# Performance work log

Hardware: AMD Instinct MI355X
Metric: run time of the kernel (lower is better)

Reference implementation:

```python
import jax, jax.numpy as jnp
import numpy as np

T, B, D, H, O = 512, 64, 512, 1024, 512

def _xavier(key, shape):
    fan_out, fan_in = shape
    limit = np.sqrt(6.0 / (fan_in + fan_out))
    return jax.random.uniform(key, shape, jnp.float32, -limit, limit)

def setup_inputs() -> dict:
    key = jax.random.key(0)
    ks = jax.random.split(key, 10)
    x = jax.random.normal(ks[0], (T, B, D), jnp.float32)
    # Gate order: i, f, o, c (stacked along first axis for a fused 4H projection;
    # math identical to 8 separate Linears in the torch module, biases init to 0
    # but we randomize them slightly for a non-trivial reference).
    Wx = jnp.concatenate([_xavier(ks[1 + g], (H, D)) for g in range(4)], axis=0)  # [4H, D]
    Wh = jnp.concatenate([_xavier(ks[5 + g], (H, H)) for g in range(4)], axis=0)  # [4H, H]
    bx = jnp.zeros((4 * H,), jnp.float32)
    bh = jnp.zeros((4 * H,), jnp.float32)
    Why = _xavier(ks[9], (O, H))
    bhy = jnp.zeros((O,), jnp.float32)
    return {"x": x, "Wx": Wx, "bx": bx, "Wh": Wh, "bh": bh, "Why": Why, "bhy": bhy}

def reference(x, Wx, bx, Wh, bh, Why, bhy):
    Hd = Wh.shape[1]
    Bd = x.shape[1]
    # Precompute all input-path projections in one batched GEMM: [T, B, 4H]
    xp = jnp.einsum('tbd,gd->tbg', x, Wx) + bx + bh

    def step(carry, xp_t):
        h, c = carry
        gates = xp_t + h @ Wh.T  # [B, 4H]
        i_t = jax.nn.sigmoid(gates[:, 0 * Hd:1 * Hd])
        f_t = jax.nn.sigmoid(gates[:, 1 * Hd:2 * Hd])
        o_t = jax.nn.sigmoid(gates[:, 2 * Hd:3 * Hd])
        c_tilde = jnp.tanh(gates[:, 3 * Hd:4 * Hd])
        c = f_t * c + i_t * c_tilde
        h = o_t * jnp.tanh(c)
        return (h, c), None

    h0 = jnp.zeros((Bd, Hd), x.dtype)
    c0 = jnp.zeros((Bd, Hd), x.dtype)
    (h, c), _ = jax.lax.scan(step, (h0, c0), xp)
    return h @ Why.T + bhy  # [B, O]
```

## Files before the change

kernel.cpp:

```cpp
#include <hip/hip_runtime.h>
#include <hip/hip_bf16.h>
#include <math.h>

constexpr int T = 512;
constexpr int B = 64;
constexpr int D = 512;
constexpr int H = 1024;
constexpr int O = 512;
constexpr int GROUPS = 2;
constexpr int BG   = B / GROUPS;
constexpr int GBLK = 128;
constexpr int COLS = 32;
constexpr int KCH  = (D + H) / 8;

typedef __attribute__((ext_vector_type(8))) __bf16 bf16x8;
typedef __attribute__((ext_vector_type(4))) float  floatx4;

struct GBar {
    unsigned arr[GBLK];
};

__global__ __launch_bounds__(256) void convert_w(
    const float* __restrict__ Wx, const float* __restrict__ Wh,
    __bf16* __restrict__ Wc)
{
    const int id = blockIdx.x * 256 + threadIdx.x;
    if (id >= GBLK * KCH * COLS) return;
    const int nl     = id & 31;
    const int kchunk = (id >> 5) % KCH;
    const int strip  = id / (KCH * COLS);
    const int s  = nl >> 4;
    const int jl = (nl >> 2) & 3;
    const int g  = nl & 3;
    const int j  = strip * 8 + 2 * jl + s;
    const int k0 = kchunk * 8;
    const float* src = (k0 < D) ? &Wx[(size_t)(g * H + j) * D + k0]
                                : &Wh[(size_t)(g * H + j) * H + (k0 - D)];
    const float4 a = *(const float4*)src;
    const float4 b = *(const float4*)(src + 4);
    __bf16 t8[8] = {(__bf16)a.x,(__bf16)a.y,(__bf16)a.z,(__bf16)a.w,
                    (__bf16)b.x,(__bf16)b.y,(__bf16)b.z,(__bf16)b.w};
    *(uint4*)&Wc[(size_t)id * 8] = *(uint4*)t8;
}

__global__ __launch_bounds__(256) void make_bias(
    const float* __restrict__ bx, const float* __restrict__ bh,
    float* __restrict__ bias)
{
    const int n = blockIdx.x * 256 + threadIdx.x;
    if (n < 4 * H) {
        const int gbn = n >> 5, nl = n & 31;
        const int s  = nl >> 4;
        const int jl = (nl >> 2) & 3;
        const int g  = nl & 3;
        const int j  = gbn * 8 + 2 * jl + s;
        bias[n] = bx[g * H + j] + bh[g * H + j];
    }
}

__global__ __launch_bounds__(128, 1) void lstm_persistent(
    const float* __restrict__ x,
    const __bf16* __restrict__ Wc,
    const float* __restrict__ bias,
    __bf16* __restrict__ hbufs,
    float* __restrict__ hfin,
    GBar* bars)
{
    __shared__ __attribute__((aligned(16))) __bf16 wlds[KCH * COLS * 8];

    const int tid   = threadIdx.x;
    const int wid   = tid >> 6;
    const int lane  = tid & 63;
    const int cm    = lane & 15;
    const int q     = lane >> 4;
    const int group = blockIdx.x >> 7;
    const int gb    = blockIdx.x & 127;
    const int n0    = gb * COLS;
    GBar* bar = bars + group;
    __bf16* hb0 = hbufs + (size_t)group * 2 * BG * H;
    __bf16* hb1 = hb0 + BG * H;

    {
        const uint4* wsrc = (const uint4*)(Wc + (size_t)gb * KCH * COLS * 8);
        uint4* wdst = (uint4*)wlds;
        for (int i = tid; i < KCH * COLS; i += 128) wdst[i] = wsrc[i];
    }
    const int p4 = cm & 3;
    const int jl = cm >> 2;
    const int row_l = wid * 16 + q * 4 + p4;
    const float4 bias0q = *(const float4*)&bias[n0 + jl * 4];
    const float4 bias1q = *(const float4*)&bias[n0 + 16 + jl * 4];
    float c0 = 0.f, c1 = 0.f;
    __syncthreads();

    const int grow = group * BG + wid * 16 + cm;
    const float* xrow = x + (size_t)grow * D + q * 8;
    const int    hoff = (wid * 16 + cm) * H + q * 8;
    const __bf16* wl  = wlds + (q * 32 + cm) * 8;
    const unsigned* fa = bar->arr + 2 * lane;

    floatx4 acc[2][2];
    float4  xcur[16][2];

    auto loadx = [&](int tt) {
        const float* xr = xrow + (size_t)tt * (B * D);
        #pragma unroll
        for (int s = 0; s < 16; ++s) {
            xcur[s][0] = *(const float4*)(xr + s * 32);
            xcur[s][1] = *(const float4*)(xr + s * 32 + 4);
        }
    };
    auto xmfma = [&]() {
        acc[0][0] = (floatx4){0,0,0,0}; acc[0][1] = (floatx4){0,0,0,0};
        acc[1][0] = (floatx4){0,0,0,0}; acc[1][1] = (floatx4){0,0,0,0};
        #pragma unroll
        for (int s = 0; s < 16; ++s) {
            const float4 a0 = xcur[s][0], a1 = xcur[s][1];
            const bf16x8 af = {(__bf16)a0.x,(__bf16)a0.y,(__bf16)a0.z,(__bf16)a0.w,
                               (__bf16)a1.x,(__bf16)a1.y,(__bf16)a1.z,(__bf16)a1.w};
            const bf16x8 b0 = *(const bf16x8*)(wl + s * 1024);
            const bf16x8 b1 = *(const bf16x8*)(wl + s * 1024 + 128);
            acc[0][s & 1] = __builtin_amdgcn_mfma_f32_16x16x32_bf16(af, b0, acc[0][s & 1], 0, 0, 0);
            acc[1][s & 1] = __builtin_amdgcn_mfma_f32_16x16x32_bf16(af, b1, acc[1][s & 1], 0, 0, 0);
        }
    };

    auto quadT = [&](float v[4]) {
        float w0 = __shfl_xor(v[1], 1), w1 = __shfl_xor(v[0], 1);
        float w2 = __shfl_xor(v[3], 1), w3 = __shfl_xor(v[2], 1);
        if (p4 & 1) { v[0] = w0; v[2] = w2; } else { v[1] = w1; v[3] = w3; }
        w0 = __shfl_xor(v[2], 2); w1 = __shfl_xor(v[3], 2);
        w2 = __shfl_xor(v[0], 2); w3 = __shfl_xor(v[1], 2);
        if (p4 & 2) { v[0] = w0; v[1] = w1; } else { v[2] = w2; v[3] = w3; }
    };

    loadx(0);
    xmfma();

    for (int t = 0; t < T; ++t) {
        const __bf16* hcur = (t & 1) ? hb1 : hb0;
        __bf16*       hnxt = (t & 1) ? hb0 : hb1;

        {
            const __bf16* hbase = hcur + hoff;
            uint4 hv[32];
            unsigned f0t, f1t;
            asm volatile(
                "1: global_load_dword %[f0], %[fa], off sc0 sc1\n\t"
                "global_load_dword %[f1], %[fa], off offset:4 sc0 sc1\n\t"
                "s_waitcnt vmcnt(0)\n\t"
                "v_min_i32 %[f0], %[f0], %[f1]\n\t"
                "v_cmp_gt_i32 vcc, %[tt], %[f0]\n\t"
                "s_cbranch_vccz 2f\n\t"
                "s_sleep 1\n\t"
                "s_branch 1b\n\t"
                "2: global_load_dwordx4 %[h0], %[hb], off sc0 sc1\n\t"
                "global_load_dwordx4 %[h1], %[hb], off offset:64 sc0 sc1\n\t"
                "global_load_dwordx4 %[h2], %[hb], off offset:128 sc0 sc1\n\t"
                "global_load_dwordx4 %[h3], %[hb], off offset:192 sc0 sc1\n\t"
                "global_load_dwordx4 %[h4], %[hb], off offset:256 sc0 sc1\n\t"
                "global_load_dwordx4 %[h5], %[hb], off offset:320 sc0 sc1\n\t"
                "global_load_dwordx4 %[h6], %[hb], off offset:384 sc0 sc1\n\t"
                "global_load_dwordx4 %[h7], %[hb], off offset:448 sc0 sc1\n\t"
                "global_load_dwordx4 %[h8], %[hb], off offset:512 sc0 sc1\n\t"
                "global_load_dwordx4 %[h9], %[hb], off offset:576 sc0 sc1\n\t"
                "global_load_dwordx4 %[h10], %[hb], off offset:640 sc0 sc1\n\t"
                "global_load_dwordx4 %[h11], %[hb], off offset:704 sc0 sc1\n\t"
                "global_load_dwordx4 %[h12], %[hb], off offset:768 sc0 sc1\n\t"
                "global_load_dwordx4 %[h13], %[hb], off offset:832 sc0 sc1\n\t"
                "global_load_dwordx4 %[h14], %[hb], off offset:896 sc0 sc1\n\t"
                "global_load_dwordx4 %[h15], %[hb], off offset:960 sc0 sc1\n\t"
                "global_load_dwordx4 %[h16], %[hb], off offset:1024 sc0 sc1\n\t"
                "global_load_dwordx4 %[h17], %[hb], off offset:1088 sc0 sc1\n\t"
                "global_load_dwordx4 %[h18], %[hb], off offset:1152 sc0 sc1\n\t"
                "global_load_dwordx4 %[h19], %[hb], off offset:1216 sc0 sc1\n\t"
                "global_load_dwordx4 %[h20], %[hb], off offset:1280 sc0 sc1\n\t"
                "global_load_dwordx4 %[h21], %[hb], off offset:1344 sc0 sc1\n\t"
                "global_load_dwordx4 %[h22], %[hb], off offset:1408 sc0 sc1\n\t"
                "global_load_dwordx4 %[h23], %[hb], off offset:1472 sc0 sc1\n\t"
                "global_load_dwordx4 %[h24], %[hb], off offset:1536 sc0 sc1\n\t"
                "global_load_dwordx4 %[h25], %[hb], off offset:1600 sc0 sc1\n\t"
                "global_load_dwordx4 %[h26], %[hb], off offset:1664 sc0 sc1\n\t"
                "global_load_dwordx4 %[h27], %[hb], off offset:1728 sc0 sc1\n\t"
                "global_load_dwordx4 %[h28], %[hb], off offset:1792 sc0 sc1\n\t"
                "global_load_dwordx4 %[h29], %[hb], off offset:1856 sc0 sc1\n\t"
                "global_load_dwordx4 %[h30], %[hb], off offset:1920 sc0 sc1\n\t"
                "global_load_dwordx4 %[h31], %[hb], off offset:1984 sc0 sc1\n\t"
                "s_waitcnt vmcnt(0)"
                : [h0]"=&v"(hv[0]),  [h1]"=&v"(hv[1]),  [h2]"=&v"(hv[2]),  [h3]"=&v"(hv[3]),
                  [h4]"=&v"(hv[4]),  [h5]"=&v"(hv[5]),  [h6]"=&v"(hv[6]),  [h7]"=&v"(hv[7]),
                  [h8]"=&v"(hv[8]),  [h9]"=&v"(hv[9]),  [h10]"=&v"(hv[10]), [h11]"=&v"(hv[11]),
                  [h12]"=&v"(hv[12]), [h13]"=&v"(hv[13]), [h14]"=&v"(hv[14]), [h15]"=&v"(hv[15]),
                  [h16]"=&v"(hv[16]), [h17]"=&v"(hv[17]), [h18]"=&v"(hv[18]), [h19]"=&v"(hv[19]),
                  [h20]"=&v"(hv[20]), [h21]"=&v"(hv[21]), [h22]"=&v"(hv[22]), [h23]"=&v"(hv[23]),
                  [h24]"=&v"(hv[24]), [h25]"=&v"(hv[25]), [h26]"=&v"(hv[26]), [h27]"=&v"(hv[27]),
                  [h28]"=&v"(hv[28]), [h29]"=&v"(hv[29]), [h30]"=&v"(hv[30]), [h31]"=&v"(hv[31]),
                  [f0]"=&v"(f0t), [f1]"=&v"(f1t)
                : [hb]"v"(hbase), [fa]"v"(fa), [tt]"v"(t)
                : "memory", "vcc");
            #pragma unroll
            for (int sg = 0; sg < 32; ++sg) {
                union { uint4 u; bf16x8 v; } hf; hf.u = hv[sg];
                const bf16x8 b0 = *(const bf16x8*)(wl + 16384 + sg * 1024);
                const bf16x8 b1 = *(const bf16x8*)(wl + 16384 + sg * 1024 + 128);
                acc[0][sg & 1] = __builtin_amdgcn_mfma_f32_16x16x32_bf16(hf.v, b0, acc[0][sg & 1], 0, 0, 0);
                acc[1][sg & 1] = __builtin_amdgcn_mfma_f32_16x16x32_bf16(hf.v, b1, acc[1][sg & 1], 0, 0, 0);
            }
        }
        const floatx4 av0 = acc[0][0] + acc[0][1];
        const floatx4 av1 = acc[1][0] + acc[1][1];

        float g0v[4] = {av0.x, av0.y, av0.z, av0.w};
        float g1v[4] = {av1.x, av1.y, av1.z, av1.w};
        quadT(g0v);
        quadT(g1v);

        if (t + 1 < T) loadx(t + 1);

        const float i0 = 1.f / (1.f + expf(-(g0v[0] + bias0q.x)));
        const float f0 = 1.f / (1.f + expf(-(g0v[1] + bias0q.y)));
        const float o0 = 1.f / (1.f + expf(-(g0v[2] + bias0q.z)));
        const float t0 = tanhf(g0v[3] + bias0q.w);
        const float i1 = 1.f / (1.f + expf(-(g1v[0] + bias1q.x)));
        const float f1 = 1.f / (1.f + expf(-(g1v[1] + bias1q.y)));
        const float o1 = 1.f / (1.f + expf(-(g1v[2] + bias1q.z)));
        const float t1 = tanhf(g1v[3] + bias1q.w);
        c0 = f0 * c0 + i0 * t0;
        c1 = f1 * c1 + i1 * t1;
        const float hv0 = o0 * tanhf(c0);
        const float hv1 = o1 * tanhf(c1);
        const int j0 = gb * 8 + 2 * jl;
        const int hi = row_l * H + j0;
        union { __bf16 h2[2]; unsigned u; } hp;
        hp.h2[0] = (__bf16)hv0; hp.h2[1] = (__bf16)hv1;
        __hip_atomic_store((unsigned*)&hnxt[hi], hp.u, __ATOMIC_RELAXED,
                           __HIP_MEMORY_SCOPE_AGENT);
        if (t == T - 1) {
            const int gr = group * BG + row_l;
            hfin[gr * H + j0]     = hv0;
            hfin[gr * H + j0 + 1] = hv1;
        }

        __syncthreads();

        if (tid == 0)
            __hip_atomic_store(&bar->arr[gb], (unsigned)(t + 1),
                               __ATOMIC_RELAXED, __HIP_MEMORY_SCOPE_AGENT);

        if (t + 1 < T) xmfma();
    }
}

__global__ __launch_bounds__(256) void out_gemm(
    const float* __restrict__ h, const float* __restrict__ Why,
    const float* __restrict__ bhy, float* __restrict__ out)
{
    const int idx = blockIdx.x * 256 + threadIdx.x;
    if (idx >= B * O) return;
    const int b = idx / O;
    const int o = idx % O;
    const float4* hv = (const float4*)&h[(size_t)b * H];
    const float4* wv = (const float4*)&Why[(size_t)o * H];
    float s = 0.f;
    #pragma unroll 4
    for (int k = 0; k < H / 4; ++k) {
        const float4 a = hv[k];
        const float4 w = wv[k];
        s += a.x * w.x + a.y * w.y + a.z * w.z + a.w * w.w;
    }
    out[idx] = s + bhy[o];
}

extern "C" void kernel_launch(void* const* d_in, const int* in_sizes, int n_in,
                              void* d_out, int out_size, void* d_ws, size_t ws_size,
                              hipStream_t stream) {
    const float* x   = (const float*)d_in[0];
    const float* Wx  = (const float*)d_in[1];
    const float* bx  = (const float*)d_in[2];
    const float* Wh  = (const float*)d_in[3];
    const float* bh  = (const float*)d_in[4];
    const float* Why = (const float*)d_in[5];
    const float* bhy = (const float*)d_in[6];
    float* out = (float*)d_out;

    char* ws = (char*)d_ws;
    __bf16* Wc    = (__bf16*)ws;
    float*  bias  = (float*)(ws + 12582912);
    __bf16* hbufs = (__bf16*)(ws + 12599296);
    GBar*   bars  = (GBar*)  (ws + 12861440);
    float*  hfin  = (float*)ws;

    (void)hipMemsetAsync(ws + 12599296, 0, 262144 + 2 * sizeof(GBar), stream);
    convert_w<<<3072, 256, 0, stream>>>(Wx, Wh, Wc);
    make_bias<<<16, 256, 0, stream>>>(bx, bh, bias);

    lstm_persistent<<<GROUPS * GBLK, 128, 0, stream>>>(x, Wc, bias, hbufs,
                                                       hfin, bars);

    out_gemm<<<(B * O + 255) / 256, 256, 0, stream>>>(hfin, Why, bhy, out);
}
```

Measured before the change: 3.198 ms.

## Widen persistent LSTM blocks to 64 columns, keep only Wh in LDS

Halves the number of persistent blocks per group (128 to 64) and doubles the hidden columns each block owns, so each h tile loaded per step feeds four MFMAs instead of two. Only the recurrent Wh slice (128 KB) is kept in LDS, and the input-projection weights are read from global memory each step. The barrier poll drops to one flag per lane and h is stored as 64-bit packed bf16. The final fp32 h copy is removed and the output GEMM reads the bf16 ping-pong buffer instead, which trades precision for skipping that write. Risks include global weight traffic in xmfma, higher per-block work, and the output reading a bf16 rather than fp32 hidden state.

```diff
diff --git a/kernel.cpp b/kernel.cpp
--- a/kernel.cpp
+++ b/kernel.cpp
@@ -9,8 +9,8 @@
 constexpr int O = 512;
 constexpr int GROUPS = 2;
 constexpr int BG   = B / GROUPS;
-constexpr int GBLK = 128;
-constexpr int COLS = 32;
+constexpr int GBLK = 64;
+constexpr int COLS = 64;
 constexpr int KCH  = (D + H) / 8;
 
 typedef __attribute__((ext_vector_type(8))) __bf16 bf16x8;
@@ -25,14 +25,14 @@
     __bf16* __restrict__ Wc)
 {
     const int id = blockIdx.x * 256 + threadIdx.x;
-    if (id >= GBLK * KCH * COLS) return;
-    const int nl     = id & 31;
-    const int kchunk = (id >> 5) % KCH;
-    const int strip  = id / (KCH * COLS);
-    const int s  = nl >> 4;
-    const int jl = (nl >> 2) & 3;
-    const int g  = nl & 3;
-    const int j  = strip * 8 + 2 * jl + s;
+    if (id >= GBLK * KCH * 64) return;
+    const int nl6    = id & 63;
+    const int kchunk = (id >> 6) % KCH;
+    const int blk    = id / (KCH * 64);
+    const int s  = nl6 >> 4;
+    const int jl = (nl6 >> 2) & 3;
+    const int g  = nl6 & 3;
+    const int j  = blk * 16 + jl * 4 + s;
     const int k0 = kchunk * 8;
     const float* src = (k0 < D) ? &Wx[(size_t)(g * H + j) * D + k0]
                                 : &Wh[(size_t)(g * H + j) * H + (k0 - D)];
@@ -49,11 +49,11 @@
 {
     const int n = blockIdx.x * 256 + threadIdx.x;
     if (n < 4 * H) {
-        const int gbn = n >> 5, nl = n & 31;
-        const int s  = nl >> 4;
-        const int jl = (nl >> 2) & 3;
-        const int g  = nl & 3;
-        const int j  = gbn * 8 + 2 * jl + s;
+        const int gbn = n >> 6, nl6 = n & 63;
+        const int s  = nl6 >> 4;
+        const int jl = (nl6 >> 2) & 3;
+        const int g  = nl6 & 3;
+        const int j  = gbn * 16 + jl * 4 + s;
         bias[n] = bx[g * H + j] + bh[g * H + j];
     }
 }
@@ -63,43 +63,45 @@
     const __bf16* __restrict__ Wc,
     const float* __restrict__ bias,
     __bf16* __restrict__ hbufs,
-    float* __restrict__ hfin,
     GBar* bars)
 {
-    __shared__ __attribute__((aligned(16))) __bf16 wlds[KCH * COLS * 8];
+    __shared__ __attribute__((aligned(16))) __bf16 wlds[128 * 512];
 
     const int tid   = threadIdx.x;
     const int wid   = tid >> 6;
     const int lane  = tid & 63;
     const int cm    = lane & 15;
     const int q     = lane >> 4;
-    const int group = blockIdx.x >> 7;
-    const int gb    = blockIdx.x & 127;
+    const int group = blockIdx.x >> 6;
+    const int gb    = blockIdx.x & 63;
     const int n0    = gb * COLS;
     GBar* bar = bars + group;
     __bf16* hb0 = hbufs + (size_t)group * 2 * BG * H;
     __bf16* hb1 = hb0 + BG * H;
 
     {
-        const uint4* wsrc = (const uint4*)(Wc + (size_t)gb * KCH * COLS * 8);
+        const uint4* wsrc = (const uint4*)(Wc + ((size_t)gb * KCH + 64) * 512);
         uint4* wdst = (uint4*)wlds;
-        for (int i = tid; i < KCH * COLS; i += 128) wdst[i] = wsrc[i];
+        for (int i = tid; i < 8192; i += 128) wdst[i] = wsrc[i];
     }
     const int p4 = cm & 3;
     const int jl = cm >> 2;
     const int row_l = wid * 16 + q * 4 + p4;
-    const float4 bias0q = *(const float4*)&bias[n0 + jl * 4];
-    const float4 bias1q = *(const float4*)&bias[n0 + 16 + jl * 4];
-    float c0 = 0.f, c1 = 0.f;
+    float4 biasq[4];
+    #pragma unroll
+    for (int s = 0; s < 4; ++s)
+        biasq[s] = *(const float4*)&bias[n0 + s * 16 + jl * 4];
+    float cst[4] = {0.f, 0.f, 0.f, 0.f};
     __syncthreads();
 
     const int grow = group * BG + wid * 16 + cm;
     const float* xrow = x + (size_t)grow * D + q * 8;
     const int    hoff = (wid * 16 + cm) * H + q * 8;
-    const __bf16* wl  = wlds + (q * 32 + cm) * 8;
-    const unsigned* fa = bar->arr + 2 * lane;
-
-    floatx4 acc[2][2];
+    const __bf16* wl  = wlds + q * 512 + cm * 8;
+    const __bf16* wxg = Wc + (size_t)gb * KCH * 512 + q * 512 + cm * 8;
+    const unsigned* fa = bar->arr + lane;
+
+    floatx4 acc[4];
     float4  xcur[16][2];
 
     auto loadx = [&](int tt) {
@@ -111,17 +113,18 @@
         }
     };
     auto xmfma = [&]() {
-        acc[0][0] = (floatx4){0,0,0,0}; acc[0][1] = (floatx4){0,0,0,0};
-        acc[1][0] = (floatx4){0,0,0,0}; acc[1][1] = (floatx4){0,0,0,0};
+        acc[0] = (floatx4){0,0,0,0}; acc[1] = (floatx4){0,0,0,0};
+        acc[2] = (floatx4){0,0,0,0}; acc[3] = (floatx4){0,0,0,0};
         #pragma unroll
-        for (int s = 0; s < 16; ++s) {
-            const float4 a0 = xcur[s][0], a1 = xcur[s][1];
+        for (int s16 = 0; s16 < 16; ++s16) {
+            const float4 a0 = xcur[s16][0], a1 = xcur[s16][1];
             const bf16x8 af = {(__bf16)a0.x,(__bf16)a0.y,(__bf16)a0.z,(__bf16)a0.w,
                                (__bf16)a1.x,(__bf16)a1.y,(__bf16)a1.z,(__bf16)a1.w};
-            const bf16x8 b0 = *(const bf16x8*)(wl + s * 1024);
-            const bf16x8 b1 = *(const bf16x8*)(wl + s * 1024 + 128);
-            acc[0][s & 1] = __builtin_amdgcn_mfma_f32_16x16x32_bf16(af, b0, acc[0][s & 1], 0, 0, 0);
-            acc[1][s & 1] = __builtin_amdgcn_mfma_f32_16x16x32_bf16(af, b1, acc[1][s & 1], 0, 0, 0);
+            #pragma unroll
+            for (int s = 0; s < 4; ++s) {
+                const bf16x8 b = *(const bf16x8*)(wxg + s16 * 2048 + s * 128);
+                acc[s] = __builtin_amdgcn_mfma_f32_16x16x32_bf16(af, b, acc[s], 0, 0, 0);
+            }
         }
     };
 
@@ -144,12 +147,10 @@
         {
             const __bf16* hbase = hcur + hoff;
             uint4 hv[32];
-            unsigned f0t, f1t;
+            unsigned f0t;
             asm volatile(
                 "1: global_load_dword %[f0], %[fa], off sc0 sc1\n\t"
-                "global_load_dword %[f1], %[fa], off offset:4 sc0 sc1\n\t"
                 "s_waitcnt vmcnt(0)\n\t"
-                "v_min_i32 %[f0], %[f0], %[f1]\n\t"
                 "v_cmp_gt_i32 vcc, %[tt], %[f0]\n\t"
                 "s_cbranch_vccz 2f\n\t"
                 "s_sleep 1\n\t"
@@ -195,51 +196,46 @@
                   [h20]"=&v"(hv[20]), [h21]"=&v"(hv[21]), [h22]"=&v"(hv[22]), [h23]"=&v"(hv[23]),
                   [h24]"=&v"(hv[24]), [h25]"=&v"(hv[25]), [h26]"=&v"(hv[26]), [h27]"=&v"(hv[27]),
                   [h28]"=&v"(hv[28]), [h29]"=&v"(hv[29]), [h30]"=&v"(hv[30]), [h31]"=&v"(hv[31]),
-                  [f0]"=&v"(f0t), [f1]"=&v"(f1t)
+                  [f0]"=&v"(f0t)
                 : [hb]"v"(hbase), [fa]"v"(fa), [tt]"v"(t)
                 : "memory", "vcc");
             #pragma unroll
             for (int sg = 0; sg < 32; ++sg) {
                 union { uint4 u; bf16x8 v; } hf; hf.u = hv[sg];
-                const bf16x8 b0 = *(const bf16x8*)(wl + 16384 + sg * 1024);
-                const bf16x8 b1 = *(const bf16x8*)(wl + 16384 + sg * 1024 + 128);
-                acc[0][sg & 1] = __builtin_amdgcn_mfma_f32_16x16x32_bf16(hf.v, b0, acc[0][sg & 1], 0, 0, 0);
-                acc[1][sg & 1] = __builtin_amdgcn_mfma_f32_16x16x32_bf16(hf.v, b1, acc[1][sg & 1], 0, 0, 0);
+                #pragma unroll
+                for (int s = 0; s < 4; ++s) {
+                    const bf16x8 b = *(const bf16x8*)(wl + sg * 2048 + s * 128);
+                    acc[s] = __builtin_amdgcn_mfma_f32_16x16x32_bf16(hf.v, b, acc[s], 0, 0, 0);
+                }
             }
         }
-        const floatx4 av0 = acc[0][0] + acc[0][1];
-        const floatx4 av1 = acc[1][0] + acc[1][1];
-
-        float g0v[4] = {av0.x, av0.y, av0.z, av0.w};
-        float g1v[4] = {av1.x, av1.y, av1.z, av1.w};
-        quadT(g0v);
-        quadT(g1v);
+
+        float gv[4][4];
+        #pragma unroll
+        for (int s = 0; s < 4; ++s) {
+            gv[s][0] = acc[s].x; gv[s][1] = acc[s].y;
+            gv[s][2] = acc[s].z; gv[s][3] = acc[s].w;
+            quadT(gv[s]);
+        }
 
         if (t + 1 < T) loadx(t + 1);
 
-        const float i0 = 1.f / (1.f + expf(-(g0v[0] + bias0q.x)));
-        const float f0 = 1.f / (1.f + expf(-(g0v[1] + bias0q.y)));
-        const float o0 = 1.f / (1.f + expf(-(g0v[2] + bias0q.z)));
-        const float t0 = tanhf(g0v[3] + bias0q.w);
-        const float i1 = 1.f / (1.f + expf(-(g1v[0] + bias1q.x)));
-        const float f1 = 1.f / (1.f + expf(-(g1v[1] + bias1q.y)));
-        const float o1 = 1.f / (1.f + expf(-(g1v[2] + bias1q.z)));
-        const float t1 = tanhf(g1v[3] + bias1q.w);
-        c0 = f0 * c0 + i0 * t0;
-        c1 = f1 * c1 + i1 * t1;
-        const float hv0 = o0 * tanhf(c0);
-        const float hv1 = o1 * tanhf(c1);
-        const int j0 = gb * 8 + 2 * jl;
+        __bf16 hq[4];
+        #pragma unroll
+        for (int s = 0; s < 4; ++s) {
+            const float ig = 1.f / (1.f + expf(-(gv[s][0] + biasq[s].x)));
+            const float fg = 1.f / (1.f + expf(-(gv[s][1] + biasq[s].y)));
+            const float og = 1.f / (1.f + expf(-(gv[s][2] + biasq[s].z)));
+            const float ct = tanhf(gv[s][3] + biasq[s].w);
+            cst[s] = fg * cst[s] + ig * ct;
+            hq[s] = (__bf16)(og * tanhf(cst[s]));
+        }
+        const int j0 = gb * 16 + jl * 4;
         const int hi = row_l * H + j0;
-        union { __bf16 h2[2]; unsigned u; } hp;
-        hp.h2[0] = (__bf16)hv0; hp.h2[1] = (__bf16)hv1;
-        __hip_atomic_store((unsigned*)&hnxt[hi], hp.u, __ATOMIC_RELAXED,
-                           __HIP_MEMORY_SCOPE_AGENT);
-        if (t == T - 1) {
-            const int gr = group * BG + row_l;
-            hfin[gr * H + j0]     = hv0;
-            hfin[gr * H + j0 + 1] = hv1;
-        }
+        union { __bf16 h4[4]; unsigned long long u; } hp;
+        hp.h4[0] = hq[0]; hp.h4[1] = hq[1]; hp.h4[2] = hq[2]; hp.h4[3] = hq[3];
+        __hip_atomic_store((unsigned long long*)&hnxt[hi], hp.u,
+                           __ATOMIC_RELAXED, __HIP_MEMORY_SCOPE_AGENT);
 
         __syncthreads();
 
@@ -252,21 +248,27 @@
 }
 
 __global__ __launch_bounds__(256) void out_gemm(
-    const float* __restrict__ h, const float* __restrict__ Why,
+    const __bf16* __restrict__ hbufs, const float* __restrict__ Why,
     const float* __restrict__ bhy, float* __restrict__ out)
 {
     const int idx = blockIdx.x * 256 + threadIdx.x;
     if (idx >= B * O) return;
     const int b = idx / O;
     const int o = idx % O;
-    const float4* hv = (const float4*)&h[(size_t)b * H];
+    const int group = b >> 5, row_l = b & 31;
+    const __bf16* hb = hbufs + (size_t)group * 2 * BG * H + (size_t)row_l * H;
     const float4* wv = (const float4*)&Why[(size_t)o * H];
     float s = 0.f;
     #pragma unroll 4
-    for (int k = 0; k < H / 4; ++k) {
-        const float4 a = hv[k];
-        const float4 w = wv[k];
-        s += a.x * w.x + a.y * w.y + a.z * w.z + a.w * w.w;
+    for (int k8 = 0; k8 < H / 8; ++k8) {
+        union { uint4 u; bf16x8 v; } hh;
+        hh.u = ((const uint4*)hb)[k8];
+        const float4 w0 = wv[2 * k8];
+        const float4 w1 = wv[2 * k8 + 1];
+        s += (float)hh.v[0] * w0.x + (float)hh.v[1] * w0.y +
+             (float)hh.v[2] * w0.z + (float)hh.v[3] * w0.w +
+             (float)hh.v[4] * w1.x + (float)hh.v[5] * w1.y +
+             (float)hh.v[6] * w1.z + (float)hh.v[7] * w1.w;
     }
     out[idx] = s + bhy[o];
 }
@@ -288,14 +290,13 @@
     float*  bias  = (float*)(ws + 12582912);
     __bf16* hbufs = (__bf16*)(ws + 12599296);
     GBar*   bars  = (GBar*)  (ws + 12861440);
-    float*  hfin  = (float*)ws;
 
     (void)hipMemsetAsync(ws + 12599296, 0, 262144 + 2 * sizeof(GBar), stream);
     convert_w<<<3072, 256, 0, stream>>>(Wx, Wh, Wc);
     make_bias<<<16, 256, 0, stream>>>(bx, bh, bias);
 
     lstm_persistent<<<GROUPS * GBLK, 128, 0, stream>>>(x, Wc, bias, hbufs,
-                                                       hfin, bars);
-
-    out_gemm<<<(B * O + 255) / 256, 256, 0, stream>>>(hfin, Why, bhy, out);
-}
+                                                       bars);
+
+    out_gemm<<<(B * O + 255) / 256, 256, 0, stream>>>(hbufs, Why, bhy, out);
+}
```

New measurement: 8.778 ms. 2.75x slower.

## Elect per-XCD leader block to poll barrier and relay readiness locally

Applied to the files above, without the earlier changes.

One block per XCD and group becomes a leader. Only the leaders poll the global step barrier, then they acquire-fence and publish a per-XCD flag. The other blocks on that XCD spin on the flag, and then load h with sc0 only, so the loads can hit the XCD's L2 instead of bypassing it. The aim is to cut cross-die barrier polling traffic and the cost of system-coherent h loads, in exchange for an extra hop in the signalling chain. Correctness depends on the non-leader's sc0 loads seeing fresh h data in L2 after the leader's fence, which may not be guaranteed without invalidation.

```diff
diff --git a/kernel.cpp b/kernel.cpp
--- a/kernel.cpp
+++ b/kernel.cpp
@@ -64,9 +64,12 @@
     const float* __restrict__ bias,
     __bf16* __restrict__ hbufs,
     float* __restrict__ hfin,
-    GBar* bars)
+    GBar* bars,
+    unsigned* invFlag,
+    unsigned* xcdCnt)
 {
     __shared__ __attribute__((aligned(16))) __bf16 wlds[KCH * COLS * 8];
+    __shared__ int sLead, sSlot;
 
     const int tid   = threadIdx.x;
     const int wid   = tid >> 6;
@@ -80,10 +83,18 @@
     __bf16* hb0 = hbufs + (size_t)group * 2 * BG * H;
     __bf16* hb1 = hb0 + BG * H;
 
+    unsigned xcd;
+    asm volatile("s_getreg_b32 %0, hwreg(HW_REG_XCC_ID)" : "=s"(xcd));
+
     {
         const uint4* wsrc = (const uint4*)(Wc + (size_t)gb * KCH * COLS * 8);
         uint4* wdst = (uint4*)wlds;
         for (int i = tid; i < KCH * COLS; i += 128) wdst[i] = wsrc[i];
+    }
+    if (tid == 0) {
+        const int slot = ((int)(xcd & 7)) * 2 + group;
+        sSlot = slot;
+        sLead = (atomicAdd(&xcdCnt[slot], 1u) == 0);
     }
     const int p4 = cm & 3;
     const int jl = cm >> 2;
@@ -92,6 +103,8 @@
     const float4 bias1q = *(const float4*)&bias[n0 + 16 + jl * 4];
     float c0 = 0.f, c1 = 0.f;
     __syncthreads();
+    const int isLead = sLead;
+    unsigned* ivf = invFlag + sSlot * 16;
 
     const int grow = group * BG + wid * 16 + cm;
     const float* xrow = x + (size_t)grow * D + q * 8;
@@ -140,10 +153,9 @@
     for (int t = 0; t < T; ++t) {
         const __bf16* hcur = (t & 1) ? hb1 : hb0;
         __bf16*       hnxt = (t & 1) ? hb0 : hb1;
-
-        {
-            const __bf16* hbase = hcur + hoff;
-            uint4 hv[32];
+        const __bf16* hbase = hcur + hoff;
+
+        if (isLead) {
             unsigned f0t, f1t;
             asm volatile(
                 "1: global_load_dword %[f0], %[fa], off sc0 sc1\n\t"
@@ -154,38 +166,64 @@
                 "s_cbranch_vccz 2f\n\t"
                 "s_sleep 1\n\t"
                 "s_branch 1b\n\t"
-                "2: global_load_dwordx4 %[h0], %[hb], off sc0 sc1\n\t"
-                "global_load_dwordx4 %[h1], %[hb], off offset:64 sc0 sc1\n\t"
-                "global_load_dwordx4 %[h2], %[hb], off offset:128 sc0 sc1\n\t"
-                "global_load_dwordx4 %[h3], %[hb], off offset:192 sc0 sc1\n\t"
-                "global_load_dwordx4 %[h4], %[hb], off offset:256 sc0 sc1\n\t"
-                "global_load_dwordx4 %[h5], %[hb], off offset:320 sc0 sc1\n\t"
-                "global_load_dwordx4 %[h6], %[hb], off offset:384 sc0 sc1\n\t"
-                "global_load_dwordx4 %[h7], %[hb], off offset:448 sc0 sc1\n\t"
-                "global_load_dwordx4 %[h8], %[hb], off offset:512 sc0 sc1\n\t"
-                "global_load_dwordx4 %[h9], %[hb], off offset:576 sc0 sc1\n\t"
-                "global_load_dwordx4 %[h10], %[hb], off offset:640 sc0 sc1\n\t"
-                "global_load_dwordx4 %[h11], %[hb], off offset:704 sc0 sc1\n\t"
-                "global_load_dwordx4 %[h12], %[hb], off offset:768 sc0 sc1\n\t"
-                "global_load_dwordx4 %[h13], %[hb], off offset:832 sc0 sc1\n\t"
-                "global_load_dwordx4 %[h14], %[hb], off offset:896 sc0 sc1\n\t"
-                "global_load_dwordx4 %[h15], %[hb], off offset:960 sc0 sc1\n\t"
-                "global_load_dwordx4 %[h16], %[hb], off offset:1024 sc0 sc1\n\t"
-                "global_load_dwordx4 %[h17], %[hb], off offset:1088 sc0 sc1\n\t"
-                "global_load_dwordx4 %[h18], %[hb], off offset:1152 sc0 sc1\n\t"
-                "global_load_dwordx4 %[h19], %[hb], off offset:1216 sc0 sc1\n\t"
-                "global_load_dwordx4 %[h20], %[hb], off offset:1280 sc0 sc1\n\t"
-                "global_load_dwordx4 %[h21], %[hb], off offset:1344 sc0 sc1\n\t"
-                "global_load_dwordx4 %[h22], %[hb], off offset:1408 sc0 sc1\n\t"
-                "global_load_dwordx4 %[h23], %[hb], off offset:1472 sc0 sc1\n\t"
-                "global_load_dwordx4 %[h24], %[hb], off offset:1536 sc0 sc1\n\t"
-                "global_load_dwordx4 %[h25], %[hb], off offset:1600 sc0 sc1\n\t"
-                "global_load_dwordx4 %[h26], %[hb], off offset:1664 sc0 sc1\n\t"
-                "global_load_dwordx4 %[h27], %[hb], off offset:1728 sc0 sc1\n\t"
-                "global_load_dwordx4 %[h28], %[hb], off offset:1792 sc0 sc1\n\t"
-                "global_load_dwordx4 %[h29], %[hb], off offset:1856 sc0 sc1\n\t"
-                "global_load_dwordx4 %[h30], %[hb], off offset:1920 sc0 sc1\n\t"
-                "global_load_dwordx4 %[h31], %[hb], off offset:1984 sc0 sc1\n\t"
+                "2:"
+                : [f0]"=&v"(f0t), [f1]"=&v"(f1t)
+                : [fa]"v"(fa), [tt]"v"(t)
+                : "memory", "vcc");
+            __builtin_amdgcn_fence(__ATOMIC_ACQUIRE, "agent");
+            if (tid == 0)
+                __hip_atomic_store(&ivf[0], (unsigned)(t + 1),
+                                   __ATOMIC_RELAXED, __HIP_MEMORY_SCOPE_AGENT);
+        } else {
+            unsigned f0t;
+            asm volatile(
+                "1: global_load_dword %[f0], %[iv], off sc0 sc1\n\t"
+                "s_waitcnt vmcnt(0)\n\t"
+                "v_cmp_gt_u32 vcc, %[t1], %[f0]\n\t"
+                "s_cbranch_vccz 2f\n\t"
+                "s_sleep 1\n\t"
+                "s_branch 1b\n\t"
+                "2:"
+                : [f0]"=&v"(f0t)
+                : [iv]"v"(ivf), [t1]"v"(t + 1)
+                : "memory", "vcc");
+        }
+
+        {
+            uint4 hv[32];
+            asm volatile(
+                "global_load_dwordx4 %[h0], %[hb], off sc0\n\t"
+                "global_load_dwordx4 %[h1], %[hb], off offset:64 sc0\n\t"
+                "global_load_dwordx4 %[h2], %[hb], off offset:128 sc0\n\t"
+                "global_load_dwordx4 %[h3], %[hb], off offset:192 sc0\n\t"
+                "global_load_dwordx4 %[h4], %[hb], off offset:256 sc0\n\t"
+                "global_load_dwordx4 %[h5], %[hb], off offset:320 sc0\n\t"
+                "global_load_dwordx4 %[h6], %[hb], off offset:384 sc0\n\t"
+                "global_load_dwordx4 %[h7], %[hb], off offset:448 sc0\n\t"
+                "global_load_dwordx4 %[h8], %[hb], off offset:512 sc0\n\t"
+                "global_load_dwordx4 %[h9], %[hb], off offset:576 sc0\n\t"
+                "global_load_dwordx4 %[h10], %[hb], off offset:640 sc0\n\t"
+                "global_load_dwordx4 %[h11], %[hb], off offset:704 sc0\n\t"
+                "global_load_dwordx4 %[h12], %[hb], off offset:768 sc0\n\t"
+                "global_load_dwordx4 %[h13], %[hb], off offset:832 sc0\n\t"
+                "global_load_dwordx4 %[h14], %[hb], off offset:896 sc0\n\t"
+                "global_load_dwordx4 %[h15], %[hb], off offset:960 sc0\n\t"
+                "global_load_dwordx4 %[h16], %[hb], off offset:1024 sc0\n\t"
+                "global_load_dwordx4 %[h17], %[hb], off offset:1088 sc0\n\t"
+                "global_load_dwordx4 %[h18], %[hb], off offset:1152 sc0\n\t"
+                "global_load_dwordx4 %[h19], %[hb], off offset:1216 sc0\n\t"
+                "global_load_dwordx4 %[h20], %[hb], off offset:1280 sc0\n\t"
+                "global_load_dwordx4 %[h21], %[hb], off offset:1344 sc0\n\t"
+                "global_load_dwordx4 %[h22], %[hb], off offset:1408 sc0\n\t"
+                "global_load_dwordx4 %[h23], %[hb], off offset:1472 sc0\n\t"
+                "global_load_dwordx4 %[h24], %[hb], off offset:1536 sc0\n\t"
+                "global_load_dwordx4 %[h25], %[hb], off offset:1600 sc0\n\t"
+                "global_load_dwordx4 %[h26], %[hb], off offset:1664 sc0\n\t"
+                "global_load_dwordx4 %[h27], %[hb], off offset:1728 sc0\n\t"
+                "global_load_dwordx4 %[h28], %[hb], off offset:1792 sc0\n\t"
+                "global_load_dwordx4 %[h29], %[hb], off offset:1856 sc0\n\t"
+                "global_load_dwordx4 %[h30], %[hb], off offset:1920 sc0\n\t"
+                "global_load_dwordx4 %[h31], %[hb], off offset:1984 sc0\n\t"
                 "s_waitcnt vmcnt(0)"
                 : [h0]"=&v"(hv[0]),  [h1]"=&v"(hv[1]),  [h2]"=&v"(hv[2]),  [h3]"=&v"(hv[3]),
                   [h4]"=&v"(hv[4]),  [h5]"=&v"(hv[5]),  [h6]"=&v"(hv[6]),  [h7]"=&v"(hv[7]),
@@ -194,10 +232,9 @@
                   [h16]"=&v"(hv[16]), [h17]"=&v"(hv[17]), [h18]"=&v"(hv[18]), [h19]"=&v"(hv[19]),
                   [h20]"=&v"(hv[20]), [h21]"=&v"(hv[21]), [h22]"=&v"(hv[22]), [h23]"=&v"(hv[23]),
                   [h24]"=&v"(hv[24]), [h25]"=&v"(hv[25]), [h26]"=&v"(hv[26]), [h27]"=&v"(hv[27]),
-                  [h28]"=&v"(hv[28]), [h29]"=&v"(hv[29]), [h30]"=&v"(hv[30]), [h31]"=&v"(hv[31]),
-                  [f0]"=&v"(f0t), [f1]"=&v"(f1t)
-                : [hb]"v"(hbase), [fa]"v"(fa), [tt]"v"(t)
-                : "memory", "vcc");
+                  [h28]"=&v"(hv[28]), [h29]"=&v"(hv[29]), [h30]"=&v"(hv[30]), [h31]"=&v"(hv[31])
+                : [hb]"v"(hbase)
+                : "memory");
             #pragma unroll
             for (int sg = 0; sg < 32; ++sg) {
                 union { uint4 u; bf16x8 v; } hf; hf.u = hv[sg];
@@ -284,18 +321,21 @@
     float* out = (float*)d_out;
 
     char* ws = (char*)d_ws;
-    __bf16* Wc    = (__bf16*)ws;
-    float*  bias  = (float*)(ws + 12582912);
-    __bf16* hbufs = (__bf16*)(ws + 12599296);
-    GBar*   bars  = (GBar*)  (ws + 12861440);
-    float*  hfin  = (float*)ws;
-
-    (void)hipMemsetAsync(ws + 12599296, 0, 262144 + 2 * sizeof(GBar), stream);
+    __bf16*   Wc      = (__bf16*)ws;
+    float*    bias    = (float*)(ws + 12582912);
+    __bf16*   hbufs   = (__bf16*)(ws + 12599296);
+    GBar*     bars    = (GBar*)  (ws + 12861440);
+    unsigned* invFlag = (unsigned*)(ws + 12862464);
+    unsigned* xcdCnt  = (unsigned*)(ws + 12863488);
+    float*    hfin    = (float*)ws;
+
+    (void)hipMemsetAsync(ws + 12599296, 0, 264256, stream);
     convert_w<<<3072, 256, 0, stream>>>(Wx, Wh, Wc);
     make_bias<<<16, 256, 0, stream>>>(bx, bh, bias);
 
     lstm_persistent<<<GROUPS * GBLK, 128, 0, stream>>>(x, Wc, bias, hbufs,
-                                                       hfin, bars);
+                                                       hfin, bars, invFlag,
+                                                       xcdCnt);
 
     out_gemm<<<(B * O + 255) / 256, 256, 0, stream>>>(hfin, Why, bhy, out);
 }
```

Result: slower. 3.375 ms (+5.5%).
